# Kernel optimization log

Hardware: AMD Instinct MI355X
Metric: run time of the kernel (lower is better)

## Reference

```python
import jax, jax.numpy as jnp
import numpy as np

B, T, C, H = 4, 2048, 1024, 16
HD = C // H  # head_dim = 64


def _rope(x, cos, sin):
    # x: [B,H,T,HD]; cos/sin: [T,HD//2] -> broadcast [1,1,T,HD//2]
    x1 = x[..., 0::2]
    x2 = x[..., 1::2]
    cos = cos[None, None]
    sin = sin[None, None]
    o1 = x1 * cos - x2 * sin
    o2 = x1 * sin + x2 * cos
    # interleave back to [..., HD]
    return jnp.stack([o1, o2], axis=-1).reshape(x.shape)


def setup_inputs() -> dict:
    key = jax.random.key(0)
    ks = jax.random.split(key, 10)
    x = jax.random.normal(ks[0], (B, T, C), jnp.float32)
    # rotary frequencies (llama-style, theta=10000), stored as (cos,sin)
    inv_freq = 1.0 / (10000.0 ** (jnp.arange(0, HD, 2, dtype=jnp.float32) / HD))
    freqs = jnp.outer(jnp.arange(T, dtype=jnp.float32), inv_freq)  # [T, HD/2]
    freqs_cis = jnp.stack([jnp.cos(freqs), jnp.sin(freqs)], axis=-1)  # [T, HD/2, 2]
    attn_mask = jnp.tril(jnp.ones((T, T), jnp.int32))  # causal
    padding_mask = jnp.ones((B, T), jnp.int32)
    w = 0.02
    Wq = jax.random.normal(ks[1], (C, C), jnp.float32) * w
    Wk = jax.random.normal(ks[2], (C, C), jnp.float32) * w
    Wv = jax.random.normal(ks[3], (C, C), jnp.float32) * w
    Wp = jax.random.normal(ks[4], (C, C), jnp.float32) * w
    bq = jnp.zeros((C,), jnp.float32)
    bk = jnp.zeros((C,), jnp.float32)
    bv = jnp.zeros((C,), jnp.float32)
    bp = jnp.zeros((C,), jnp.float32)
    return {"x": x, "freqs_cis": freqs_cis, "attn_mask": attn_mask,
            "padding_mask": padding_mask, "Wq": Wq, "bq": bq, "Wk": Wk,
            "bk": bk, "Wv": Wv, "bv": bv, "Wp": Wp, "bp": bp}


def reference(x, freqs_cis, attn_mask, padding_mask, Wq, bq, Wk, bk, Wv, bv, Wp, bp):
    b, t, c = x.shape
    # qkv projections -> [B,H,T,HD]
    def heads(y):
        return y.reshape(b, t, H, HD).transpose(0, 2, 1, 3)
    q = heads(x @ Wq.T + bq)
    k = heads(x @ Wk.T + bk)
    v = heads(x @ Wv.T + bv)
    cos, sin = freqs_cis[..., 0], freqs_cis[..., 1]  # [T, HD/2]
    q = _rope(q, cos, sin)
    k = _rope(k, cos, sin)
    att = jnp.einsum('bhqd,bhkd->bhqk', q, k) * (1.0 / np.sqrt(HD).astype(np.float32))
    att = jnp.where(attn_mask[None, None] == 0, -1e30, att)
    att = jnp.where(padding_mask[:, None, None, :] == 0, -1e30, att)
    att = jax.nn.softmax(att, axis=-1)
    # dropout omitted (eval mode / deterministic reference)
    y = jnp.einsum('bhqk,bhkd->bhqd', att, v)
    y = y.transpose(0, 2, 1, 3).reshape(b, t, c)
    return y @ Wp.T + bp
```

## Files before the change

### kernel.cpp

```cpp
#include <hip/hip_runtime.h>
#include <hip/hip_bf16.h>

#define TB 2048
#define CC 1024
#define NH 16
#define HD 64
#define NB 4
#define BHX (NB*NH)
#define BTX (NB*TB)

typedef __attribute__((ext_vector_type(8))) short bf16x8;
typedef __attribute__((ext_vector_type(4))) float f32x4;
typedef __attribute__((ext_vector_type(4))) unsigned short us4;

__device__ __forceinline__ unsigned short bfb(float f) {
  __hip_bfloat16 h = __float2bfloat16(f);
  return __builtin_bit_cast(unsigned short, h);
}
__device__ __forceinline__ float fexp2(float x) {
  return __builtin_amdgcn_exp2f(x);
}
template <int CTRL>
__device__ __forceinline__ float dppf(float x) {
  int r = __builtin_amdgcn_update_dpp(0, __builtin_bit_cast(int, x), CTRL, 0xf, 0xf, false);
  return __builtin_bit_cast(float, r);
}

__device__ __forceinline__ void gld_lds16(const void* g, void* l) {
  __builtin_amdgcn_global_load_lds(
      (const __attribute__((address_space(1))) unsigned*)g,
      (__attribute__((address_space(3))) unsigned*)l, 16, 0, 0);
}

__global__ void cvt_f32_bf16(const float* __restrict__ src,
                             unsigned short* __restrict__ dst, int n4) {
  int i = blockIdx.x * blockDim.x + threadIdx.x;
  if (i >= n4) return;
  f32x4 v = ((const f32x4*)src)[i];
  us4 o;
#pragma unroll
  for (int j = 0; j < 4; j++) o[j] = bfb(v[j]);
  ((us4*)dst)[i] = o;
}

__global__ void cvt_w4(const float* __restrict__ s0, const float* __restrict__ s1,
                       const float* __restrict__ s2, const float* __restrict__ s3,
                       unsigned short* __restrict__ d0, unsigned short* __restrict__ d1,
                       unsigned short* __restrict__ d2, unsigned short* __restrict__ d3) {
  int y = blockIdx.y;
  const float* s = y == 0 ? s0 : y == 1 ? s1 : y == 2 ? s2 : s3;
  unsigned short* d = y == 0 ? d0 : y == 1 ? d1 : y == 2 ? d2 : d3;
  int i = blockIdx.x * 256 + threadIdx.x;
  f32x4 v = ((const f32x4*)s)[i];
  us4 o;
#pragma unroll
  for (int j = 0; j < 4; j++) o[j] = bfb(v[j]);
  ((us4*)d)[i] = o;
}

__global__ void prep_bias(const float* __restrict__ bq, const float* __restrict__ bk,
                          const float* __restrict__ bv, float* __restrict__ out) {
  int i = blockIdx.x * 256 + threadIdx.x;
  float v = i < 1024 ? bq[i] : i < 2048 ? bk[i - 1024] : bv[i - 2048];
  out[i] = v;
}

template <int MODE>
__global__ __launch_bounds__(512) void gemm8(
    const unsigned short* __restrict__ A, const unsigned short* __restrict__ Bw,
    const float* __restrict__ bias, const float* __restrict__ fcg,
    void* __restrict__ Cout, int N, int nbx)
{
  const int K = 1024;
  __shared__ __align__(16) unsigned short As[3][16384];
  __shared__ __align__(16) unsigned short Bs[3][8192];
  const int tid = threadIdx.x;
  const int lane = tid & 63, wid = tid >> 6;
  const int g = lane >> 4, l4 = lane & 15;
  const int wr = wid >> 1, wc = wid & 1;
  const int cpx = gridDim.x >> 3;
  const int swz = (blockIdx.x & 7) * cpx + (blockIdx.x >> 3);
  const int bx = swz % nbx, by = swz / nbx;
  const int brow = by * 256, bcol = bx * 128;

  const unsigned short* asrc[4];
  int adst[4];
#pragma unroll
  for (int s = 0; s < 4; s++) {
    int cid = tid + 512 * s;
    int row = cid >> 3, sc = (cid & 7) ^ (row & 7);
    asrc[s] = A + (size_t)(brow + row) * K + sc * 8;
    adst[s] = cid * 8;
  }
  const unsigned short* bsrc[2];
  int bdst[2];
#pragma unroll
  for (int s = 0; s < 2; s++) {
    int cid = tid + 512 * s;
    int row = cid >> 3, sc = (cid & 7) ^ (row & 7);
    bsrc[s] = Bw + (size_t)(bcol + row) * K + sc * 8;
    bdst[s] = cid * 8;
  }

  int ar[4], br[4];
#pragma unroll
  for (int i = 0; i < 4; i++) {
    ar[i] = (wr * 64 + i * 16 + l4) * 64;
    br[i] = (wc * 64 + i * 16 + l4) * 64;
  }
  const int sl0 = ((g) ^ (l4 & 7)) * 8;
  const int sl1 = ((4 + g) ^ (l4 & 7)) * 8;

  f32x4 acc[4][4] = {};

#pragma unroll
  for (int s = 0; s < 4; s++) gld_lds16(asrc[s], &As[0][adst[s]]);
#pragma unroll
  for (int s = 0; s < 2; s++) gld_lds16(bsrc[s], &Bs[0][bdst[s]]);
#pragma unroll
  for (int s = 0; s < 4; s++) gld_lds16(asrc[s] + 64, &As[1][adst[s]]);
#pragma unroll
  for (int s = 0; s < 2; s++) gld_lds16(bsrc[s] + 64, &Bs[1][bdst[s]]);
  asm volatile("s_waitcnt vmcnt(6)" ::: "memory");
  __builtin_amdgcn_s_barrier();
  __builtin_amdgcn_sched_barrier(0);

  const int nt = K >> 6;
  int c = 0;
  for (int t = 0; t < nt; t++) {
    const unsigned short* Ac = As[c];
    const unsigned short* Bc = Bs[c];
    {
      bf16x8 af[4], bf[4];
#pragma unroll
      for (int mf = 0; mf < 4; mf++) af[mf] = *(const bf16x8*)&Ac[ar[mf] + sl0];
#pragma unroll
      for (int nf = 0; nf < 4; nf++) bf[nf] = *(const bf16x8*)&Bc[br[nf] + sl0];
      __builtin_amdgcn_s_setprio(1);
#pragma unroll
      for (int mf = 0; mf < 4; mf++)
#pragma unroll
        for (int nf = 0; nf < 4; nf++)
          acc[mf][nf] = __builtin_amdgcn_mfma_f32_16x16x32_bf16(af[mf], bf[nf], acc[mf][nf], 0, 0, 0);
      __builtin_amdgcn_s_setprio(0);
      asm volatile("" ::: "memory");
      __builtin_amdgcn_s_barrier();
      __builtin_amdgcn_sched_barrier(0);
    }
    {
      if (t + 2 < nt) {
        int c2 = c + 2; if (c2 >= 3) c2 -= 3;
        const int ko = (t + 2) << 6;
#pragma unroll
        for (int s = 0; s < 4; s++) gld_lds16(asrc[s] + ko, &As[c2][adst[s]]);
#pragma unroll
        for (int s = 0; s < 2; s++) gld_lds16(bsrc[s] + ko, &Bs[c2][bdst[s]]);
      }
      bf16x8 af[4], bf[4];
#pragma unroll
      for (int mf = 0; mf < 4; mf++) af[mf] = *(const bf16x8*)&Ac[ar[mf] + sl1];
#pragma unroll
      for (int nf = 0; nf < 4; nf++) bf[nf] = *(const bf16x8*)&Bc[br[nf] + sl1];
      __builtin_amdgcn_s_setprio(1);
#pragma unroll
      for (int mf = 0; mf < 4; mf++)
#pragma unroll
        for (int nf = 0; nf < 4; nf++)
          acc[mf][nf] = __builtin_amdgcn_mfma_f32_16x16x32_bf16(af[mf], bf[nf], acc[mf][nf], 0, 0, 0);
      __builtin_amdgcn_s_setprio(0);
      if (t + 2 < nt)
        asm volatile("s_waitcnt vmcnt(6)" ::: "memory");
      else if (t + 1 < nt)
        asm volatile("s_waitcnt vmcnt(0)" ::: "memory");
      if (t + 1 < nt) {
        asm volatile("" ::: "memory");
        __builtin_amdgcn_s_barrier();
        __builtin_amdgcn_sched_barrier(0);
      }
    }
    c = (c == 2) ? 0 : c + 1;
  }

#pragma unroll
  for (int mf = 0; mf < 4; mf++) {
    int grow0 = brow + wr * 64 + mf * 16 + 4 * g;
#pragma unroll
    for (int nf = 0; nf < 4; nf++) {
      int gcol = bcol + wc * 64 + nf * 16 + l4;
      float bv = bias[gcol];
      if (MODE == 0) {
        float* out = (float*)Cout;
#pragma unroll
        for (int r = 0; r < 4; r++)
          out[(size_t)(grow0 + r) * N + gcol] = acc[mf][nf][r] + bv;
      } else {
        unsigned short* out = (unsigned short*)Cout;
        int part = gcol >> 10;
        int cc2 = gcol & 1023;
        int h = cc2 >> 6, d = cc2 & 63;
        int dbase = d & ~1;
        float sgn = (d & 1) ? 1.f : -1.f;
        bool isqk = (part < 2);
#pragma unroll
        for (int r = 0; r < 4; r++) {
          int grow = grow0 + r;
          int b = grow >> 11, tt = grow & 2047;
          float v = acc[mf][nf][r] + bv;
          float w = __shfl_xor(v, 1, 64);
          float o = v;
          if (isqk) {
            float cth = fcg[(size_t)tt * 64 + dbase];
            float sth = fcg[(size_t)tt * 64 + dbase + 1];
            o = v * cth + sgn * w * sth;
          }
          size_t dst = (size_t)part * ((size_t)BHX * TB * HD)
                     + ((size_t)(b * NH + h) * TB + tt) * HD + d;
          out[dst] = bfb(o);
        }
      }
    }
  }
}

__global__ void transpose_v(const unsigned short* __restrict__ v,
                            unsigned short* __restrict__ vT) {
  int bh = blockIdx.y, t0 = blockIdx.x * 64;
  __shared__ __align__(16) unsigned short tile[64][72];
  int tid = threadIdx.x;
#pragma unroll
  for (int s = 0; s < 2; s++) {
    int cid = tid + 256 * s;
    int r = cid >> 3, c8 = (cid & 7) * 8;
    bf16x8 val = *(const bf16x8*)(v + ((size_t)bh * TB + t0 + r) * HD + c8);
    *(bf16x8*)&tile[r][c8] = val;
  }
  __syncthreads();
#pragma unroll
  for (int s = 0; s < 2; s++) {
    int cid = tid + 256 * s;
    int rr = cid >> 3, cc = (cid & 7) * 8;
    bf16x8 o;
#pragma unroll
    for (int i = 0; i < 8; i++) o[i] = (short)tile[cc + i][rr];
    *(bf16x8*)(vT + ((size_t)bh * HD + rr) * TB + t0 + cc) = o;
  }
}

__global__ __launch_bounds__(256, 4) void flash_fwd(
    const unsigned short* __restrict__ q, const unsigned short* __restrict__ k,
    const unsigned short* __restrict__ vT, unsigned short* __restrict__ yb)
{
  __shared__ __align__(16) unsigned short Ks[2][4096];
  __shared__ __align__(16) unsigned short Vs[2][4096];
  __shared__ __align__(16) unsigned short Ps[4][16][64];

  const int tid = threadIdx.x, wid = tid >> 6, lane = tid & 63;
  const int g = lane >> 4, l4 = lane & 15;

  const int b = blockIdx.x;
  const int xcd = b & 7;
  const int idx = b >> 3;
  const int bh = (xcd << 3) | (idx & 7);
  const int p = idx >> 3;

  const int off0 = tid << 4;
  const int row0 = off0 >> 7, sc0 = ((off0 >> 4) & 7) ^ (row0 & 7);
  const int off1 = off0 + 4096;
  const int row1 = off1 >> 7, sc1 = ((off1 >> 4) & 7) ^ (row1 & 7);
  const int koff0 = (row0 << 6) + (sc0 << 3);
  const int koff1 = (row1 << 6) + (sc1 << 3);
  const int voff0 = (row0 << 11) + (sc0 << 3);
  const int voff1 = (row1 << 11) + (sc1 << 3);

  const float SCL2 = 0.18033688011112042f;

  const unsigned short* kb = k  + ((size_t)bh << 17);
  const unsigned short* vb = vT + ((size_t)bh << 17);

#pragma unroll 1
  for (int sel = 0; sel < 2; sel++) {
    const int q64 = sel ? (31 - p) : p;
    const int rbase = q64 * 64 + wid * 16;

    bf16x8 qf0, qf1;
    {
      const unsigned short* qp = q + (((size_t)bh * TB + rbase + l4) << 6);
      qf0 = *(const bf16x8*)(qp + g * 8);
      qf1 = *(const bf16x8*)(qp + 32 + g * 8);
    }

    float m_run[4], l_run[4];
    f32x4 acc_o[4] = {};
#pragma unroll
    for (int j = 0; j < 4; j++) { m_run[j] = -1e30f; l_run[j] = 0.f; }

    gld_lds16(kb + koff0, &Ks[0][off0 >> 1]);
    gld_lds16(kb + koff1, &Ks[0][off1 >> 1]);
    gld_lds16(vb + voff0, &Vs[0][off0 >> 1]);
    gld_lds16(vb + voff1, &Vs[0][off1 >> 1]);
    __syncthreads();

    for (int kt = 0; kt <= q64; kt++) {
      const int cur = kt & 1;
      if (kt < q64) {
        const int kadd = (kt + 1) << 12;
        const int vadd = (kt + 1) << 6;
        gld_lds16(kb + koff0 + kadd, &Ks[cur ^ 1][off0 >> 1]);
        gld_lds16(kb + koff1 + kadd, &Ks[cur ^ 1][off1 >> 1]);
        gld_lds16(vb + voff0 + vadd, &Vs[cur ^ 1][off0 >> 1]);
        gld_lds16(vb + voff1 + vadd, &Vs[cur ^ 1][off1 >> 1]);
      }
      const unsigned short* Kc = Ks[cur];
      const unsigned short* Vc = Vs[cur];

      float sv[4][4];
      __builtin_amdgcn_s_setprio(1);
#pragma unroll
      for (int cb = 0; cb < 4; cb++) {
        const int r = cb * 16 + l4;
        const int sw = (r & 7) * 8;
        bf16x8 kb0 = *(const bf16x8*)&Kc[r * 64 + ((g * 8) ^ sw)];
        bf16x8 kb1 = *(const bf16x8*)&Kc[r * 64 + (((g + 4) * 8) ^ sw)];
        f32x4 z = {0.f, 0.f, 0.f, 0.f};
        z = __builtin_amdgcn_mfma_f32_16x16x32_bf16(qf0, kb0, z, 0, 0, 0);
        z = __builtin_amdgcn_mfma_f32_16x16x32_bf16(qf1, kb1, z, 0, 0, 0);
#pragma unroll
        for (int j = 0; j < 4; j++)
          sv[cb][j] = z[j] * SCL2;
      }
      __builtin_amdgcn_s_setprio(0);
      if (kt == q64) {
        const int rq = wid * 16 + 4 * g;
#pragma unroll
        for (int cb = 0; cb < 4; cb++)
#pragma unroll
          for (int j = 0; j < 4; j++)
            if (cb * 16 + l4 > rq + j) sv[cb][j] = -1e30f;
      }

      float mt[4];
#pragma unroll
      for (int j = 0; j < 4; j++) {
        float m = fmaxf(fmaxf(sv[0][j], sv[1][j]), fmaxf(sv[2][j], sv[3][j]));
        m = fmaxf(m, dppf<0x121>(m));
        m = fmaxf(m, dppf<0x122>(m));
        m = fmaxf(m, dppf<0x124>(m));
        m = fmaxf(m, dppf<0x128>(m));
        mt[j] = m;
      }
      bool need = !((mt[0] <= m_run[0] + 8.f) & (mt[1] <= m_run[1] + 8.f) &
                    (mt[2] <= m_run[2] + 8.f) & (mt[3] <= m_run[3] + 8.f));
      if (__any(need)) {
#pragma unroll
        for (int j = 0; j < 4; j++) {
          float mn = fmaxf(m_run[j], mt[j]);
          float alpha = fexp2(m_run[j] - mn);
          m_run[j] = mn;
          l_run[j] *= alpha;
#pragma unroll
          for (int db = 0; db < 4; db++) acc_o[db][j] *= alpha;
        }
      }
#pragma unroll
      for (int j = 0; j < 4; j++) {
        float s0 = fexp2(sv[0][j] - m_run[j]); sv[0][j] = s0;
        float s1 = fexp2(sv[1][j] - m_run[j]); sv[1][j] = s1;
        float s2 = fexp2(sv[2][j] - m_run[j]); sv[2][j] = s2;
        float s3 = fexp2(sv[3][j] - m_run[j]); sv[3][j] = s3;
        float p2 = (s0 + s1) + (s2 + s3);
        p2 += dppf<0x121>(p2);
        p2 += dppf<0x122>(p2);
        p2 += dppf<0x124>(p2);
        p2 += dppf<0x128>(p2);
        l_run[j] += p2;
      }

#pragma unroll
      for (int cb = 0; cb < 4; cb++)
#pragma unroll
        for (int j = 0; j < 4; j++) {
          const int xch = (cb * 2 + (l4 >> 3)) ^ ((g & 1) * 4 + j);
          Ps[wid][4 * g + j][xch * 8 + (l4 & 7)] = bfb(sv[cb][j]);
        }
      asm volatile("s_waitcnt lgkmcnt(0)" ::: "memory");
      __builtin_amdgcn_sched_barrier(0);
      bf16x8 pa0 = *(const bf16x8*)&Ps[wid][l4][(g ^ (l4 & 7)) * 8];
      bf16x8 pa1 = *(const bf16x8*)&Ps[wid][l4][((4 + g) ^ (l4 & 7)) * 8];
      __builtin_amdgcn_s_setprio(1);
#pragma unroll
      for (int db = 0; db < 4; db++) {
        const int r = db * 16 + l4;
        const int sw = (r & 7) * 8;
        bf16x8 vb0 = *(const bf16x8*)&Vc[r * 64 + ((g * 8) ^ sw)];
        bf16x8 vb1 = *(const bf16x8*)&Vc[r * 64 + (((g + 4) * 8) ^ sw)];
        acc_o[db] = __builtin_amdgcn_mfma_f32_16x16x32_bf16(pa0, vb0, acc_o[db], 0, 0, 0);
        acc_o[db] = __builtin_amdgcn_mfma_f32_16x16x32_bf16(pa1, vb1, acc_o[db], 0, 0, 0);
      }
      __builtin_amdgcn_s_setprio(0);
      __syncthreads();
    }

    unsigned short* yp = yb + ((size_t)(bh >> 4) * TB) * CC + (size_t)(bh & 15) * HD;
    const int qr0 = rbase + 4 * g;
    float inv[4];
#pragma unroll
    for (int j = 0; j < 4; j++) inv[j] = 1.0f / l_run[j];
#pragma unroll
    for (int db = 0; db < 4; db++) {
      const int d = db * 16 + l4;
#pragma unroll
      for (int j = 0; j < 4; j++)
        yp[(size_t)(qr0 + j) * CC + d] = bfb(acc_o[db][j] * inv[j]);
    }
  }
}

extern "C" void kernel_launch(void* const* d_in, const int* in_sizes, int n_in,
                              void* d_out, int out_size, void* d_ws, size_t ws_size,
                              hipStream_t stream) {
  (void)in_sizes; (void)n_in; (void)out_size; (void)ws_size;
  const float* x  = (const float*)d_in[0];
  const float* fc = (const float*)d_in[1];
  const float* Wq = (const float*)d_in[4];
  const float* bq = (const float*)d_in[5];
  const float* Wk = (const float*)d_in[6];
  const float* bk = (const float*)d_in[7];
  const float* Wv = (const float*)d_in[8];
  const float* bv = (const float*)d_in[9];
  const float* Wp = (const float*)d_in[10];
  const float* bp = (const float*)d_in[11];

  char* ws = (char*)d_ws;
  unsigned short* xb   = (unsigned short*)(ws + 0);
  unsigned short* wqkv = (unsigned short*)(ws + 16777216);
  unsigned short* wp   = (unsigned short*)(ws + 23068672);
  float*          bqkv = (float*)(ws + 25165824);
  unsigned short* qkv  = (unsigned short*)(ws + 25182208);
  unsigned short* vT   = qkv + 3 * (size_t)8388608;
  unsigned short* yb   = xb;

  cvt_f32_bf16<<<(2097152 + 255) / 256, 256, 0, stream>>>(x, xb, 2097152);
  cvt_w4<<<dim3(1024, 4), 256, 0, stream>>>(Wq, Wk, Wv, Wp,
      wqkv, wqkv + 1048576, wqkv + 2097152, wp);
  prep_bias<<<dim3(12), 256, 0, stream>>>(bq, bk, bv, bqkv);

  gemm8<1><<<dim3(768), 512, 0, stream>>>(xb, wqkv, bqkv, fc, qkv, 3072, 24);
  transpose_v<<<dim3(32, 64), 256, 0, stream>>>(qkv + 2 * (size_t)8388608, vT);
  flash_fwd<<<dim3(1024), 256, 0, stream>>>(qkv, qkv + (size_t)8388608, vT, yb);
  gemm8<0><<<dim3(256), 512, 0, stream>>>(yb, wp, bp, nullptr, (float*)d_out, 1024, 8);
}
```

Baseline: 241.6 us.

## Switch GEMM to double-buffered LDS with four-phase ping-pong barrier schedule

The projection GEMM goes from a three-stage LDS ring prefetching two tiles ahead to a two-buffer scheme that prefetches one tile ahead. The global-to-LDS loads for the next tile are spread across four sub-phases, and each sub-phase issues half of the M fragments' MFMAs between workgroup barriers. The smaller LDS footprint may let more workgroups fit per CU, and the phased barriers resemble a ping-pong schedule that keeps waves interleaved. In exchange there is less prefetch distance to hide latency, many more barriers per K step, and a full vmcnt(0) wait at the end of each tile.

```diff
diff --git a/kernel.cpp b/kernel.cpp
--- a/kernel.cpp
+++ b/kernel.cpp
@@ -72,8 +72,8 @@
     void* __restrict__ Cout, int N, int nbx)
 {
   const int K = 1024;
-  __shared__ __align__(16) unsigned short As[3][16384];
-  __shared__ __align__(16) unsigned short Bs[3][8192];
+  __shared__ __align__(16) unsigned short As[2][16384];
+  __shared__ __align__(16) unsigned short Bs[2][8192];
   const int tid = threadIdx.x;
   const int lane = tid & 63, wid = tid >> 6;
   const int g = lane >> 4, l4 = lane & 15;
@@ -108,8 +108,7 @@
     ar[i] = (wr * 64 + i * 16 + l4) * 64;
     br[i] = (wc * 64 + i * 16 + l4) * 64;
   }
-  const int sl0 = ((g) ^ (l4 & 7)) * 8;
-  const int sl1 = ((4 + g) ^ (l4 & 7)) * 8;
+  const int sl[2] = { ((g) ^ (l4 & 7)) * 8, ((4 + g) ^ (l4 & 7)) * 8 };
 
   f32x4 acc[4][4] = {};
 
@@ -117,68 +116,55 @@
   for (int s = 0; s < 4; s++) gld_lds16(asrc[s], &As[0][adst[s]]);
 #pragma unroll
   for (int s = 0; s < 2; s++) gld_lds16(bsrc[s], &Bs[0][bdst[s]]);
-#pragma unroll
-  for (int s = 0; s < 4; s++) gld_lds16(asrc[s] + 64, &As[1][adst[s]]);
-#pragma unroll
-  for (int s = 0; s < 2; s++) gld_lds16(bsrc[s] + 64, &Bs[1][bdst[s]]);
-  asm volatile("s_waitcnt vmcnt(6)" ::: "memory");
+  asm volatile("s_waitcnt vmcnt(0)" ::: "memory");
   __builtin_amdgcn_s_barrier();
   __builtin_amdgcn_sched_barrier(0);
 
   const int nt = K >> 6;
-  int c = 0;
   for (int t = 0; t < nt; t++) {
+    const int c = t & 1;
     const unsigned short* Ac = As[c];
     const unsigned short* Bc = Bs[c];
-    {
-      bf16x8 af[4], bf[4];
-#pragma unroll
-      for (int mf = 0; mf < 4; mf++) af[mf] = *(const bf16x8*)&Ac[ar[mf] + sl0];
-#pragma unroll
-      for (int nf = 0; nf < 4; nf++) bf[nf] = *(const bf16x8*)&Bc[br[nf] + sl0];
+    const bool more = (t + 1 < nt);
+    const int ko = (t + 1) << 6;
+#pragma unroll
+    for (int p = 0; p < 4; p++) {
+      const int h = p >> 1, mfp = (p & 1) * 2;
+      bf16x8 af0 = *(const bf16x8*)&Ac[ar[mfp] + sl[h]];
+      bf16x8 af1 = *(const bf16x8*)&Ac[ar[mfp + 1] + sl[h]];
+      bf16x8 bf0 = *(const bf16x8*)&Bc[br[0] + sl[h]];
+      bf16x8 bf1 = *(const bf16x8*)&Bc[br[1] + sl[h]];
+      bf16x8 bf2 = *(const bf16x8*)&Bc[br[2] + sl[h]];
+      bf16x8 bf3 = *(const bf16x8*)&Bc[br[3] + sl[h]];
+      if (more) {
+        if (p == 0) {
+          gld_lds16(asrc[0] + ko, &As[c ^ 1][adst[0]]);
+          gld_lds16(asrc[1] + ko, &As[c ^ 1][adst[1]]);
+        } else if (p == 1) {
+          gld_lds16(asrc[2] + ko, &As[c ^ 1][adst[2]]);
+          gld_lds16(asrc[3] + ko, &As[c ^ 1][adst[3]]);
+        } else if (p == 2) {
+          gld_lds16(bsrc[0] + ko, &Bs[c ^ 1][bdst[0]]);
+          gld_lds16(bsrc[1] + ko, &Bs[c ^ 1][bdst[1]]);
+        }
+      }
+      __builtin_amdgcn_sched_barrier(0);
+      __builtin_amdgcn_s_barrier();
+      asm volatile("s_waitcnt lgkmcnt(0)" ::: "memory");
+      __builtin_amdgcn_sched_barrier(0);
       __builtin_amdgcn_s_setprio(1);
 #pragma unroll
-      for (int mf = 0; mf < 4; mf++)
-#pragma unroll
-        for (int nf = 0; nf < 4; nf++)
-          acc[mf][nf] = __builtin_amdgcn_mfma_f32_16x16x32_bf16(af[mf], bf[nf], acc[mf][nf], 0, 0, 0);
+      for (int nf = 0; nf < 4; nf++) {
+        bf16x8 b = (nf == 0) ? bf0 : (nf == 1) ? bf1 : (nf == 2) ? bf2 : bf3;
+        acc[mfp][nf]     = __builtin_amdgcn_mfma_f32_16x16x32_bf16(af0, b, acc[mfp][nf], 0, 0, 0);
+        acc[mfp + 1][nf] = __builtin_amdgcn_mfma_f32_16x16x32_bf16(af1, b, acc[mfp + 1][nf], 0, 0, 0);
+      }
       __builtin_amdgcn_s_setprio(0);
-      asm volatile("" ::: "memory");
+      if (p == 3)
+        asm volatile("s_waitcnt vmcnt(0)" ::: "memory");
+      __builtin_amdgcn_sched_barrier(0);
       __builtin_amdgcn_s_barrier();
-      __builtin_amdgcn_sched_barrier(0);
     }
-    {
-      if (t + 2 < nt) {
-        int c2 = c + 2; if (c2 >= 3) c2 -= 3;
-        const int ko = (t + 2) << 6;
-#pragma unroll
-        for (int s = 0; s < 4; s++) gld_lds16(asrc[s] + ko, &As[c2][adst[s]]);
-#pragma unroll
-        for (int s = 0; s < 2; s++) gld_lds16(bsrc[s] + ko, &Bs[c2][bdst[s]]);
-      }
-      bf16x8 af[4], bf[4];
-#pragma unroll
-      for (int mf = 0; mf < 4; mf++) af[mf] = *(const bf16x8*)&Ac[ar[mf] + sl1];
-#pragma unroll
-      for (int nf = 0; nf < 4; nf++) bf[nf] = *(const bf16x8*)&Bc[br[nf] + sl1];
-      __builtin_amdgcn_s_setprio(1);
-#pragma unroll
-      for (int mf = 0; mf < 4; mf++)
-#pragma unroll
-        for (int nf = 0; nf < 4; nf++)
-          acc[mf][nf] = __builtin_amdgcn_mfma_f32_16x16x32_bf16(af[mf], bf[nf], acc[mf][nf], 0, 0, 0);
-      __builtin_amdgcn_s_setprio(0);
-      if (t + 2 < nt)
-        asm volatile("s_waitcnt vmcnt(6)" ::: "memory");
-      else if (t + 1 < nt)
-        asm volatile("s_waitcnt vmcnt(0)" ::: "memory");
-      if (t + 1 < nt) {
-        asm volatile("" ::: "memory");
-        __builtin_amdgcn_s_barrier();
-        __builtin_amdgcn_sched_barrier(0);
-      }
-    }
-    c = (c == 2) ? 0 : c + 1;
   }
 
 #pragma unroll
```

After: 249.5 us. 3.3% more time.
